# Kernel tuning notes

Measured on AMD Instinct MI355X. Metric: run time of the kernel, lower is better.

Reference implementation:

```python
import jax, jax.numpy as jnp
import numpy as np

D_MODEL = 512
NUM_HEADS = 8
D_HEAD = D_MODEL // NUM_HEADS
QMAX = 127.0  # int8 narrow-range symmetric
EPS = 1e-8


def _quant_dequant_weight(w):
    # per-output-channel symmetric int8 quant-dequant (brevitas default style)
    s = jnp.maximum(jnp.max(jnp.abs(w), axis=1, keepdims=True) / QMAX, EPS)
    return jnp.clip(jnp.round(w / s), -QMAX, QMAX) * s


def _quant_dequant_act(x):
    # per-tensor symmetric int8 quant-dequant (QuantIdentity)
    s = jnp.maximum(jnp.max(jnp.abs(x)) / QMAX, EPS)
    return jnp.clip(jnp.round(x / s), -QMAX, QMAX) * s


def _qlinear(x, w, b):
    return jnp.einsum('btd,od->bto', x, _quant_dequant_weight(w)) + b


def setup_inputs() -> dict:
    key = jax.random.key(0)
    ks = jax.random.split(key, 10)
    B, T = 2, 4096
    lim = 1.0 / np.sqrt(D_MODEL)
    mk = lambda k: jax.random.uniform(k, (D_MODEL, D_MODEL), jnp.float32, -lim, lim)
    mb = lambda k: jax.random.uniform(k, (D_MODEL,), jnp.float32, -lim, lim)
    return {
        'x': jax.random.normal(ks[0], (B, T, D_MODEL), jnp.float32),
        'mask': jax.random.randint(ks[1], (B, T), 0, 2, jnp.int32),
        'Wq': mk(ks[2]), 'bq': mb(ks[3]),
        'Wk': mk(ks[4]), 'bk': mb(ks[5]),
        'Wv': mk(ks[6]), 'bv': mb(ks[7]),
        'Wo': mk(ks[8]), 'bo': mb(ks[9]),
    }


def reference(x, mask, Wq, bq, Wk, bk, Wv, bv, Wo, bo):
    B, T, _ = x.shape
    shape = lambda t: t.reshape(B, T, NUM_HEADS, D_HEAD).transpose(0, 2, 1, 3)  # (B,H,T,dh)
    q = shape(_qlinear(x, Wq, bq))
    k = shape(_qlinear(x, Wk, bk))
    v = shape(_qlinear(x, Wv, bv))
    scores = jnp.einsum('bhtd,bhsd->bhts', q, k) / np.sqrt(D_HEAD)
    keep = (mask != 0)[:, None, None, :]  # (B,1,1,T), 0 = masked
    scores = jnp.where(keep, scores, -jnp.inf)
    attn = jax.nn.softmax(scores, axis=-1)
    ctx = jnp.einsum('bhts,bhsd->bhtd', attn, v)
    ctx = ctx.transpose(0, 2, 1, 3).reshape(B, T, D_MODEL)
    out = _qlinear(ctx, Wo, bo)
    return _quant_dequant_act(out)
```

## Files before the change

### kernel.cpp

```cpp
#include <hip/hip_runtime.h>
#include <hip/hip_bf16.h>

typedef __bf16 bf16;
typedef __bf16 bf16x8 __attribute__((ext_vector_type(8)));
typedef __bf16 bf16x4v __attribute__((ext_vector_type(4)));
typedef float f32x4 __attribute__((ext_vector_type(4)));

#define D_MODEL 512
#define T_SEQ   4096
#define NH      8
#define DH      64
#define M_ROWS  8192
#define VROW    8224
#define QK_SCALE 0.18033688011112042f

__device__ __forceinline__ void gload16(const void* g, void* l) {
  __builtin_amdgcn_global_load_lds(
      (const __attribute__((address_space(1))) unsigned int*)g,
      (__attribute__((address_space(3))) unsigned int*)l, 16, 0, 0);
}

#define WAITV(N) asm volatile("s_waitcnt vmcnt(" #N ")" ::: "memory")
#define CFENCE   asm volatile("" ::: "memory")

__global__ __launch_bounds__(64) void detect_dtype(const unsigned short* __restrict__ xr,
                                                   int* __restrict__ flag)
{
  int lane = threadIdx.x;
  int cnt = 0;
  for (int i = lane; i < 4096; i += 64) {
    unsigned short u = xr[i];
    int e = (u >> 7) & 0xFF;
    bool insane = (e >= 133) || (e > 0 && e <= 96) || (e == 0 && (u & 0x7F) != 0);
    cnt += insane ? 1 : 0;
  }
#pragma unroll
  for (int off = 32; off >= 1; off >>= 1) cnt += __shfl_xor(cnt, off);
  if (lane == 0) *flag = (cnt > 400) ? 1 : 0;
}

__global__ __launch_bounds__(256) void convert_x(const void* __restrict__ xr,
                                                 const int* __restrict__ flag,
                                                 bf16* __restrict__ xb, int n)
{
  int i = (blockIdx.x * blockDim.x + threadIdx.x) * 4;
  if (i >= n) return;
  if (*flag) {
    float4 v = *(const float4*)((const float*)xr + i);
    __align__(8) bf16 o[4] = {(bf16)v.x, (bf16)v.y, (bf16)v.z, (bf16)v.w};
    *(uint2*)(xb + i) = *(uint2*)o;
  } else {
    *(uint2*)(xb + i) = *(const uint2*)((const bf16*)xr + i);
  }
}

__global__ __launch_bounds__(1024) void prep_aux(
    const void* b0, const void* b1, const void* b2, const void* b3,
    const int* __restrict__ mask,
    const int* __restrict__ flag, float* __restrict__ bf, float* __restrict__ mf)
{
  const void* ps[4] = {b0, b1, b2, b3};
  int fl = *flag;
  int g = blockIdx.x * 1024 + threadIdx.x;
  if (g < 4 * D_MODEL) {
    int w = g >> 9, o = g & 511;
    bf[g] = fl ? ((const float*)ps[w])[o] : (float)((const bf16*)ps[w])[o];
  }
  mf[g] = mask[g] ? -16.0f : -1e30f;
}

__global__ __launch_bounds__(256) void qdq_weights(
    const void* __restrict__ Wq, const void* __restrict__ Wk,
    const void* __restrict__ Wv, const void* __restrict__ Wo,
    const int* __restrict__ flag, bf16* __restrict__ out)
{
  int wave = threadIdx.x >> 6, lane = threadIdx.x & 63;
  int gid = blockIdx.x * 4 + wave;
  int w = gid >> 9, row = gid & 511;
  const void* W = (w == 0) ? Wq : (w == 1) ? Wk : (w == 2) ? Wv : Wo;
  int fl = *flag;
  float v[8]; float amax = 0.f;
#pragma unroll
  for (int i = 0; i < 8; i++) {
    int idx = row * D_MODEL + lane + 64 * i;
    v[i] = fl ? ((const float*)W)[idx] : (float)((const bf16*)W)[idx];
    amax = fmaxf(amax, fabsf(v[i]));
  }
#pragma unroll
  for (int off = 32; off >= 1; off >>= 1) amax = fmaxf(amax, __shfl_xor(amax, off));
  float s = fmaxf(amax / 127.0f, 1e-8f);
  bf16* dst = out + (size_t)gid * D_MODEL;
#pragma unroll
  for (int i = 0; i < 8; i++) {
    float q = rintf(v[i] / s);
    q = fminf(fmaxf(q, -127.f), 127.f);
    dst[lane + 64*i] = (bf16)(q * s);
  }
}

__global__ __launch_bounds__(256) void gemm_qkv(
    const bf16* __restrict__ A, const bf16* __restrict__ W,
    const float* __restrict__ bias,
    bf16* __restrict__ Qh, bf16* __restrict__ Kh, bf16* __restrict__ VTP)
{
  __shared__ __align__(16) bf16 As[2][128 * 32];
  __shared__ __align__(16) bf16 Bs[2][128 * 32];

  const int tid = threadIdx.x;
  const int wave = tid >> 6, lane = tid & 63;
  const int lr = lane & 15, quad = lane >> 4;
  const int wm = (wave >> 1) * 64, wn = (wave & 1) * 64;
  const int m0 = blockIdx.x * 128, n0 = blockIdx.y * 128;
  const int sec = blockIdx.y >> 2;

  const bf16* aSrc[2]; const bf16* bSrc[2];
#pragma unroll
  for (int ii = 0; ii < 2; ii++) {
    int s = ii * 256 + tid, row = s >> 2, sl = s & 3;
    int g = (row ^ (row >> 2)) & 3;
    aSrc[ii] = A + (size_t)(m0 + row) * D_MODEL + ((sl ^ g) << 3);
    bSrc[ii] = W + (size_t)(n0 + row) * D_MODEL + ((sl ^ g) << 3);
  }

  f32x4 acc[4][4];
#pragma unroll
  for (int i = 0; i < 4; i++)
#pragma unroll
    for (int j = 0; j < 4; j++) acc[i][j] = f32x4{0.f, 0.f, 0.f, 0.f};

#pragma unroll
  for (int d = 0; d < 2; d++) {
#pragma unroll
    for (int ii = 0; ii < 2; ii++) {
      int s = ii * 256 + tid;
      gload16(aSrc[ii] + d * 32, &As[d][s * 8]);
      gload16(bSrc[ii] + d * 32, &Bs[d][s * 8]);
    }
  }
  WAITV(4);
  __builtin_amdgcn_s_barrier();
  CFENCE;

  for (int k = 0; k < 16; k++) {
    const int cur = k & 1;
    bf16x8 af[4], bfr[4];
#pragma unroll
    for (int mt = 0; mt < 4; mt++) {
      int row = wm + mt * 16 + lr;
      af[mt] = *(const bf16x8*)&As[cur][row * 32 + ((quad ^ ((row ^ (row >> 2)) & 3)) << 3)];
    }
#pragma unroll
    for (int nt = 0; nt < 4; nt++) {
      int row = wn + nt * 16 + lr;
      bfr[nt] = *(const bf16x8*)&Bs[cur][row * 32 + ((quad ^ ((row ^ (row >> 2)) & 3)) << 3)];
    }
#pragma unroll
    for (int mt = 0; mt < 4; mt++)
#pragma unroll
      for (int nt = 0; nt < 4; nt++)
        acc[mt][nt] = __builtin_amdgcn_mfma_f32_16x16x32_bf16(af[mt], bfr[nt], acc[mt][nt], 0, 0, 0);

    if (k < 15) {
      __builtin_amdgcn_s_barrier();
      CFENCE;
      if (k < 14) {
#pragma unroll
        for (int ii = 0; ii < 2; ii++) {
          int s = ii * 256 + tid;
          gload16(aSrc[ii] + (k + 2) * 32, &As[cur][s * 8]);
          gload16(bSrc[ii] + (k + 2) * 32, &Bs[cur][s * 8]);
        }
        WAITV(4);
      } else {
        WAITV(0);
      }
      __builtin_amdgcn_s_barrier();
      CFENCE;
    }
  }

  const float scale = (sec == 0) ? QK_SCALE : 1.0f;
#pragma unroll
  for (int mt = 0; mt < 4; mt++) {
    int grow = m0 + wm + mt * 16 + quad * 4;
#pragma unroll
    for (int nt = 0; nt < 4; nt++) {
      int gcol = n0 + wn + nt * 16 + lr;
      float b = bias[gcol];
      if (sec == 2) {
        bf16x4v pk;
#pragma unroll
        for (int r = 0; r < 4; r++) pk[r] = (bf16)(acc[mt][nt][r] + b);
        *(bf16x4v*)(VTP + (size_t)(gcol - 1024) * VROW + grow) = pk;
      } else {
        bf16* dst = (sec == 0) ? Qh : Kh;
        int c = gcol & 511;
        int hh = c >> 6, c64 = c & 63;
#pragma unroll
        for (int r = 0; r < 4; r++) {
          int row = grow + r;
          int bb = row >> 12, t = row & 4095;
          dst[((size_t)(bb * NH + hh) * T_SEQ + t) * DH + c64] =
              (bf16)((acc[mt][nt][r] + b) * scale);
        }
      }
    }
  }
}

__global__ __launch_bounds__(256) void gemm_o(
    const bf16* __restrict__ A, const bf16* __restrict__ W,
    const float* __restrict__ bias,
    float* __restrict__ Cf, unsigned int* __restrict__ amaxp)
{
  __shared__ __align__(16) bf16 As[2][64 * 32];
  __shared__ __align__(16) bf16 Bs[2][128 * 32];
  __shared__ float wred[4];

  const int tid = threadIdx.x;
  const int wave = tid >> 6, lane = tid & 63;
  const int lr = lane & 15, quad = lane >> 4;
  const int wm = (wave >> 1) * 32, wn = (wave & 1) * 64;
  const int m0 = blockIdx.x * 64, n0 = blockIdx.y * 128;

  const bf16* aSrc; const bf16* bSrc[2];
  {
    int s = tid, row = s >> 2, sl = s & 3;
    int g = (row ^ (row >> 2)) & 3;
    aSrc = A + (size_t)(m0 + row) * D_MODEL + ((sl ^ g) << 3);
  }
#pragma unroll
  for (int ii = 0; ii < 2; ii++) {
    int s = ii * 256 + tid, row = s >> 2, sl = s & 3;
    int g = (row ^ (row >> 2)) & 3;
    bSrc[ii] = W + (size_t)(n0 + row) * D_MODEL + ((sl ^ g) << 3);
  }

  f32x4 acc[2][4];
#pragma unroll
  for (int i = 0; i < 2; i++)
#pragma unroll
    for (int j = 0; j < 4; j++) acc[i][j] = f32x4{0.f, 0.f, 0.f, 0.f};

#pragma unroll
  for (int d = 0; d < 2; d++) {
    gload16(aSrc + d * 32, &As[d][tid * 8]);
#pragma unroll
    for (int ii = 0; ii < 2; ii++) {
      int s = ii * 256 + tid;
      gload16(bSrc[ii] + d * 32, &Bs[d][s * 8]);
    }
  }
  WAITV(3);
  __builtin_amdgcn_s_barrier();
  CFENCE;

  for (int k = 0; k < 16; k++) {
    const int cur = k & 1;
    bf16x8 af[2], bfr[4];
#pragma unroll
    for (int mt = 0; mt < 2; mt++) {
      int row = wm + mt * 16 + lr;
      af[mt] = *(const bf16x8*)&As[cur][row * 32 + ((quad ^ ((row ^ (row >> 2)) & 3)) << 3)];
    }
#pragma unroll
    for (int nt = 0; nt < 4; nt++) {
      int row = wn + nt * 16 + lr;
      bfr[nt] = *(const bf16x8*)&Bs[cur][row * 32 + ((quad ^ ((row ^ (row >> 2)) & 3)) << 3)];
    }
#pragma unroll
    for (int mt = 0; mt < 2; mt++)
#pragma unroll
      for (int nt = 0; nt < 4; nt++)
        acc[mt][nt] = __builtin_amdgcn_mfma_f32_16x16x32_bf16(af[mt], bfr[nt], acc[mt][nt], 0, 0, 0);

    if (k < 15) {
      __builtin_amdgcn_s_barrier();
      CFENCE;
      if (k < 14) {
        gload16(aSrc + (k + 2) * 32, &As[cur][tid * 8]);
#pragma unroll
        for (int ii = 0; ii < 2; ii++) {
          int s = ii * 256 + tid;
          gload16(bSrc[ii] + (k + 2) * 32, &Bs[cur][s * 8]);
        }
        WAITV(3);
      } else {
        WAITV(0);
      }
      __builtin_amdgcn_s_barrier();
      CFENCE;
    }
  }

  float lmax = 0.f;
#pragma unroll
  for (int mt = 0; mt < 2; mt++) {
    int grow = m0 + wm + mt * 16 + quad * 4;
#pragma unroll
    for (int nt = 0; nt < 4; nt++) {
      int gcol = n0 + wn + nt * 16 + lr;
      float b = bias[gcol];
#pragma unroll
      for (int r = 0; r < 4; r++) {
        float v = acc[mt][nt][r] + b;
        Cf[(size_t)(grow + r) * D_MODEL + gcol] = v;
        lmax = fmaxf(lmax, fabsf(v));
      }
    }
  }
#pragma unroll
  for (int off = 32; off >= 1; off >>= 1) lmax = fmaxf(lmax, __shfl_xor(lmax, off));
  if (lane == 0) wred[wave] = lmax;
  __syncthreads();
  if (tid == 0) {
    float m = fmaxf(fmaxf(wred[0], wred[1]), fmaxf(wred[2], wred[3]));
    atomicMax(amaxp, __float_as_uint(m));
  }
}

__global__ __launch_bounds__(256, 2) void attn(
    const bf16* __restrict__ Q, const bf16* __restrict__ K, const bf16* __restrict__ VT,
    const float* __restrict__ maskf, bf16* __restrict__ ctx)
{
  __shared__ __align__(16) bf16 Ks[3][64 * 64];
  __shared__ __align__(16) bf16 Vs[3][64 * 64];
  __shared__ __align__(16) float Mf[T_SEQ];

  const int tid = threadIdx.x;
  const int wave = tid >> 6, lane = tid & 63;
  const int lr = lane & 15, quad = lane >> 4;
  const int i = blockIdx.x;
  const int bh = (i & 7) * 2 + ((i >> 3) & 1);
  const int qb = i >> 4;
  const int b = bh >> 3, h = bh & 7;
  const int q0 = qb * 128 + wave * 32;

  const bf16* Qb = Q + (size_t)bh * T_SEQ * DH;
  const bf16* Kb = K + (size_t)bh * T_SEQ * DH;
  const bf16* Vb = VT + (size_t)(h * DH) * VROW + (size_t)b * T_SEQ;
  const float* mb = maskf + b * T_SEQ;

  const int phase = (qb * 2) & 63;

  const bf16* kSrc[2]; const bf16* vSrc[2];
#pragma unroll
  for (int ii = 0; ii < 2; ii++) {
    int s = ii * 256 + tid, row = s >> 3, sl = s & 7;
    int kt = row >> 4, m = row & 15;
    int keym = ((m >> 2) << 3) + ((kt & 1) << 2) + (m & 3) + ((kt >> 1) << 5);
    kSrc[ii] = Kb + (size_t)keym * DH + ((sl ^ (row & 7)) << 3);
    vSrc[ii] = Vb + (size_t)row * VROW + ((sl ^ (row & 7)) << 3);
  }

  bf16x8 qf[2][2];
#pragma unroll
  for (int qt = 0; qt < 2; qt++) {
    const bf16* rq = Qb + (size_t)(q0 + qt * 16 + lr) * DH;
    qf[qt][0] = *(const bf16x8*)(rq + quad * 8);
    qf[qt][1] = *(const bf16x8*)(rq + 32 + quad * 8);
  }
  WAITV(0);

#pragma unroll
  for (int ii = 0; ii < 4; ii++) {
    int g = ii * 256 + tid;
    gload16(mb + g * 4, &Mf[g * 4]);
  }
#pragma unroll
  for (int d = 0; d < 3; d++) {
    int kb = ((phase + d) & 63) * 64;
#pragma unroll
    for (int ii = 0; ii < 2; ii++) {
      int s = ii * 256 + tid;
      gload16(kSrc[ii] + (size_t)kb * DH, &Ks[d][s * 8]);
      gload16(vSrc[ii] + kb, &Vs[d][s * 8]);
    }
  }

  f32x4 O[2][4];
#pragma unroll
  for (int a = 0; a < 2; a++)
#pragma unroll
    for (int c = 0; c < 4; c++) O[a][c] = f32x4{0.f, 0.f, 0.f, 0.f};
  float lacc[2] = {0.f, 0.f};

  WAITV(8);
  __builtin_amdgcn_s_barrier();
  CFENCE;

  int cur = 0, cc = phase;
  for (int j = 0; j < 64; j++) {
    f32x4 mk[4];
#pragma unroll
    for (int kt = 0; kt < 4; kt++)
      mk[kt] = *(const f32x4*)&Mf[cc * 64 + ((kt >> 1) << 5) + (quad << 3) + ((kt & 1) << 2)];

    bf16x8 kr[4][2];
#pragma unroll
    for (int kt = 0; kt < 4; kt++)
#pragma unroll
      for (int kh = 0; kh < 2; kh++)
        kr[kt][kh] = *(const bf16x8*)&Ks[cur][(kt * 16 + lr) * 64 +
                                             (((kh * 4 + quad) ^ (lr & 7)) << 3)];

    bf16x8 pfa[2][2];
#pragma unroll
    for (int qt = 0; qt < 2; qt++) {
      f32x4 z[4];
#pragma unroll
      for (int kt = 0; kt < 4; kt++) {
        f32x4 t = mk[kt];
        t = __builtin_amdgcn_mfma_f32_16x16x32_bf16(kr[kt][0], qf[qt][0], t, 0, 0, 0);
        t = __builtin_amdgcn_mfma_f32_16x16x32_bf16(kr[kt][1], qf[qt][1], t, 0, 0, 0);
        z[kt] = t;
      }
      float la = lacc[qt];
#pragma unroll
      for (int kt = 0; kt < 4; kt++) {
#pragma unroll
        for (int r = 0; r < 4; r++) {
          float p = __builtin_amdgcn_exp2f(z[kt][r]);
          la += p;
          pfa[qt][kt >> 1][((kt & 1) << 2) + r] = (bf16)p;
        }
      }
      lacc[qt] = la;
    }

    bf16x8 vr[4][2];
#pragma unroll
    for (int nt = 0; nt < 4; nt++)
#pragma unroll
      for (int ks = 0; ks < 2; ks++)
        vr[nt][ks] = *(const bf16x8*)&Vs[cur][(nt * 16 + lr) * 64 +
                                             (((ks * 4 + quad) ^ (lr & 7)) << 3)];

#pragma unroll
    for (int nt = 0; nt < 4; nt++)
#pragma unroll
      for (int qt = 0; qt < 2; qt++) {
        O[qt][nt] = __builtin_amdgcn_mfma_f32_16x16x32_bf16(pfa[qt][0], vr[nt][0], O[qt][nt], 0, 0, 0);
        O[qt][nt] = __builtin_amdgcn_mfma_f32_16x16x32_bf16(pfa[qt][1], vr[nt][1], O[qt][nt], 0, 0, 0);
      }

    if (j < 63) {
      __builtin_amdgcn_s_barrier();
      CFENCE;
      if (j < 61) {
        int kb = ((cc + 3) & 63) * 64;
#pragma unroll
        for (int ii = 0; ii < 2; ii++) {
          int s = ii * 256 + tid;
          gload16(kSrc[ii] + (size_t)kb * DH, &Ks[cur][s * 8]);
          gload16(vSrc[ii] + kb, &Vs[cur][s * 8]);
        }
        WAITV(8);
      } else if (j == 61) {
        WAITV(4);
      } else {
        WAITV(0);
      }
      __builtin_amdgcn_s_barrier();
      CFENCE;
    }
    cur = (cur == 2) ? 0 : cur + 1;
    cc = (cc + 1) & 63;
  }

#pragma unroll
  for (int qt = 0; qt < 2; qt++) {
    float ls = lacc[qt];
    ls += __shfl_xor(ls, 16);
    ls += __shfl_xor(ls, 32);
    float linv = 1.0f / ls;
    float lO[4];
#pragma unroll
    for (int r = 0; r < 4; r++) lO[r] = __shfl(linv, quad * 4 + r);
#pragma unroll
    for (int nt = 0; nt < 4; nt++)
#pragma unroll
      for (int r = 0; r < 4; r++) {
        size_t row = (size_t)(b * T_SEQ + q0 + qt * 16 + quad * 4 + r);
        ctx[row * D_MODEL + h * DH + nt * 16 + lr] = (bf16)(O[qt][nt][r] * lO[r]);
      }
  }
}

__global__ __launch_bounds__(256) void act_qdq(
    const float* __restrict__ pre, const unsigned int* __restrict__ amaxp,
    const int* __restrict__ flag, void* __restrict__ outv, int n)
{
  int i = (blockIdx.x * blockDim.x + threadIdx.x) * 4;
  if (i >= n) return;
  float s = fmaxf(__uint_as_float(*amaxp) / 127.0f, 1e-8f);
  float4 v = *(const float4*)(pre + i);
  float o[4] = {v.x, v.y, v.z, v.w};
#pragma unroll
  for (int r = 0; r < 4; r++) {
    float q = rintf(o[r] / s);
    q = fminf(fmaxf(q, -127.f), 127.f);
    o[r] = q * s;
  }
  if (*flag) {
    *(float4*)((float*)outv + i) = make_float4(o[0], o[1], o[2], o[3]);
  } else {
    __align__(8) bf16 ob[4] = {(bf16)o[0], (bf16)o[1], (bf16)o[2], (bf16)o[3]};
    *(uint2*)((bf16*)outv + i) = *(uint2*)ob;
  }
}

extern "C" void kernel_launch(void* const* d_in, const int* in_sizes, int n_in,
                              void* d_out, int out_size, void* d_ws, size_t ws_size,
                              hipStream_t stream) {
  const void* x    = d_in[0];
  const int*  mask = (const int*)d_in[1];
  const void* Wq = d_in[2]; const void* bq = d_in[3];
  const void* Wk = d_in[4]; const void* bk = d_in[5];
  const void* Wv = d_in[6]; const void* bv = d_in[7];
  const void* Wo = d_in[8]; const void* bo = d_in[9];

  char* ws = (char*)d_ws;
  int*  flag  = (int*)(ws + 0);
  unsigned int* amax = (unsigned int*)(ws + 64);
  float* biasf = (float*)(ws + 1024);
  float* maskf = (float*)(ws + 16384);
  bf16* Wt  = (bf16*)(ws + 65536);
  bf16* xb  = (bf16*)(ws + 4194304);
  bf16* Qm  = (bf16*)(ws + 12582912);
  bf16* Km  = (bf16*)(ws + 20971520);
  bf16* VT  = (bf16*)(ws + 29360128);
  bf16* Cm  = (bf16*)(ws + 4194304);
  float* pre = (float*)(ws + 12582912);

  hipMemsetAsync(amax, 0, 4, stream);
  detect_dtype<<<1, 64, 0, stream>>>((const unsigned short*)x, flag);
  convert_x<<<4096, 256, 0, stream>>>(x, flag, xb, M_ROWS * D_MODEL);
  prep_aux<<<8, 1024, 0, stream>>>(bq, bk, bv, bo, mask, flag, biasf, maskf);
  qdq_weights<<<512, 256, 0, stream>>>(Wq, Wk, Wv, Wo, flag, Wt);
  gemm_qkv<<<dim3(64, 12), 256, 0, stream>>>(xb, Wt, biasf, Qm, Km, VT);
  attn<<<512, 256, 0, stream>>>(Qm, Km, VT, maskf, Cm);
  gemm_o<<<dim3(128, 4), 256, 0, stream>>>(Cm, Wt + 3*262144, biasf + 1536, pre, amax);
  act_qdq<<<4096, 256, 0, stream>>>(pre, amax, flag, d_out, M_ROWS * D_MODEL);
}
```

Before: 215.8 us.

## Fuse preprocessing kernels and transpose MFMA operands for vectorized Q/K stores

Merges the dtype detection, amax memset, bias/mask prep and weight quant-dequant into a single prep_all launch, where each block recomputes the dtype flag redundantly. This removes several small launches and a memset. In gemm_qkv, the Q/K sections swap the MFMA operands so each lane holds four consecutive head-dim columns, which lets the epilogue write packed 4-element bf16 stores instead of scalar ones. Every block now re-reads the first 4096 elements of x to compute the flag, which adds some redundant traffic.

Result: no change. 219.4 us (+1.7%).

```diff
diff --git a/kernel.cpp b/kernel.cpp
--- a/kernel.cpp
+++ b/kernel.cpp
@@ -23,12 +23,22 @@
 #define WAITV(N) asm volatile("s_waitcnt vmcnt(" #N ")" ::: "memory")
 #define CFENCE   asm volatile("" ::: "memory")
 
-__global__ __launch_bounds__(64) void detect_dtype(const unsigned short* __restrict__ xr,
-                                                   int* __restrict__ flag)
+__global__ __launch_bounds__(256) void prep_all(
+    const void* __restrict__ x, const int* __restrict__ mask,
+    const void* __restrict__ Wq, const void* __restrict__ Wk,
+    const void* __restrict__ Wv, const void* __restrict__ Wo,
+    const void* __restrict__ bq, const void* __restrict__ bk,
+    const void* __restrict__ bv, const void* __restrict__ bo,
+    bf16* __restrict__ out, float* __restrict__ bf, float* __restrict__ mf,
+    int* __restrict__ flag, unsigned int* __restrict__ amax)
 {
-  int lane = threadIdx.x;
+  __shared__ int wcnt[4];
+  __shared__ int sfl;
+  const int tid = threadIdx.x;
+  const unsigned short* xr = (const unsigned short*)x;
+
   int cnt = 0;
-  for (int i = lane; i < 4096; i += 64) {
+  for (int i = tid; i < 4096; i += 256) {
     unsigned short u = xr[i];
     int e = (u >> 7) & 0xFF;
     bool insane = (e >= 133) || (e > 0 && e <= 96) || (e == 0 && (u & 0x7F) != 0);
@@ -36,7 +46,52 @@
   }
 #pragma unroll
   for (int off = 32; off >= 1; off >>= 1) cnt += __shfl_xor(cnt, off);
-  if (lane == 0) *flag = (cnt > 400) ? 1 : 0;
+  if ((tid & 63) == 0) wcnt[tid >> 6] = cnt;
+  __syncthreads();
+  if (tid == 0) sfl = ((wcnt[0] + wcnt[1] + wcnt[2] + wcnt[3]) > 400) ? 1 : 0;
+  __syncthreads();
+  const int fl = sfl;
+
+  const int blk = blockIdx.x;
+  if (blk < 512) {
+    int wave = tid >> 6, lane = tid & 63;
+    int gid = blk * 4 + wave;
+    int w = gid >> 9, row = gid & 511;
+    const void* W = (w == 0) ? Wq : (w == 1) ? Wk : (w == 2) ? Wv : Wo;
+    float v[8]; float am = 0.f;
+#pragma unroll
+    for (int i = 0; i < 8; i++) {
+      int idx = row * D_MODEL + lane + 64 * i;
+      v[i] = fl ? ((const float*)W)[idx] : (float)((const bf16*)W)[idx];
+      am = fmaxf(am, fabsf(v[i]));
+    }
+#pragma unroll
+    for (int off = 32; off >= 1; off >>= 1) am = fmaxf(am, __shfl_xor(am, off));
+    float s = fmaxf(am / 127.0f, 1e-8f);
+    bf16* dst = out + (size_t)gid * D_MODEL;
+#pragma unroll
+    for (int i = 0; i < 8; i++) {
+      float q = rintf(v[i] / s);
+      q = fminf(fmaxf(q, -127.f), 127.f);
+      dst[lane + 64 * i] = (bf16)(q * s);
+    }
+  } else {
+    int ab = blk - 512;
+    int j = ab * 1024 + tid * 4;
+    int4 mv = *(const int4*)&mask[j];
+    mf[j + 0] = mv.x ? -16.0f : -1e30f;
+    mf[j + 1] = mv.y ? -16.0f : -1e30f;
+    mf[j + 2] = mv.z ? -16.0f : -1e30f;
+    mf[j + 3] = mv.w ? -16.0f : -1e30f;
+    if (ab == 0) {
+      const void* ps[4] = {bq, bk, bv, bo};
+      for (int t = tid; t < 4 * D_MODEL; t += 256) {
+        int w = t >> 9, o = t & 511;
+        bf[t] = fl ? ((const float*)ps[w])[o] : (float)((const bf16*)ps[w])[o];
+      }
+      if (tid == 0) { *flag = fl; *amax = 0u; }
+    }
+  }
 }
 
 __global__ __launch_bounds__(256) void convert_x(const void* __restrict__ xr,
@@ -54,50 +109,6 @@
   }
 }
 
-__global__ __launch_bounds__(1024) void prep_aux(
-    const void* b0, const void* b1, const void* b2, const void* b3,
-    const int* __restrict__ mask,
-    const int* __restrict__ flag, float* __restrict__ bf, float* __restrict__ mf)
-{
-  const void* ps[4] = {b0, b1, b2, b3};
-  int fl = *flag;
-  int g = blockIdx.x * 1024 + threadIdx.x;
-  if (g < 4 * D_MODEL) {
-    int w = g >> 9, o = g & 511;
-    bf[g] = fl ? ((const float*)ps[w])[o] : (float)((const bf16*)ps[w])[o];
-  }
-  mf[g] = mask[g] ? -16.0f : -1e30f;
-}
-
-__global__ __launch_bounds__(256) void qdq_weights(
-    const void* __restrict__ Wq, const void* __restrict__ Wk,
-    const void* __restrict__ Wv, const void* __restrict__ Wo,
-    const int* __restrict__ flag, bf16* __restrict__ out)
-{
-  int wave = threadIdx.x >> 6, lane = threadIdx.x & 63;
-  int gid = blockIdx.x * 4 + wave;
-  int w = gid >> 9, row = gid & 511;
-  const void* W = (w == 0) ? Wq : (w == 1) ? Wk : (w == 2) ? Wv : Wo;
-  int fl = *flag;
-  float v[8]; float amax = 0.f;
-#pragma unroll
-  for (int i = 0; i < 8; i++) {
-    int idx = row * D_MODEL + lane + 64 * i;
-    v[i] = fl ? ((const float*)W)[idx] : (float)((const bf16*)W)[idx];
-    amax = fmaxf(amax, fabsf(v[i]));
-  }
-#pragma unroll
-  for (int off = 32; off >= 1; off >>= 1) amax = fmaxf(amax, __shfl_xor(amax, off));
-  float s = fmaxf(amax / 127.0f, 1e-8f);
-  bf16* dst = out + (size_t)gid * D_MODEL;
-#pragma unroll
-  for (int i = 0; i < 8; i++) {
-    float q = rintf(v[i] / s);
-    q = fminf(fmaxf(q, -127.f), 127.f);
-    dst[lane + 64*i] = (bf16)(q * s);
-  }
-}
-
 __global__ __launch_bounds__(256) void gemm_qkv(
     const bf16* __restrict__ A, const bf16* __restrict__ W,
     const float* __restrict__ bias,
@@ -154,11 +165,19 @@
       int row = wn + nt * 16 + lr;
       bfr[nt] = *(const bf16x8*)&Bs[cur][row * 32 + ((quad ^ ((row ^ (row >> 2)) & 3)) << 3)];
     }
-#pragma unroll
-    for (int mt = 0; mt < 4; mt++)
-#pragma unroll
-      for (int nt = 0; nt < 4; nt++)
-        acc[mt][nt] = __builtin_amdgcn_mfma_f32_16x16x32_bf16(af[mt], bfr[nt], acc[mt][nt], 0, 0, 0);
+    if (sec == 2) {
+#pragma unroll
+      for (int mt = 0; mt < 4; mt++)
+#pragma unroll
+        for (int nt = 0; nt < 4; nt++)
+          acc[mt][nt] = __builtin_amdgcn_mfma_f32_16x16x32_bf16(af[mt], bfr[nt], acc[mt][nt], 0, 0, 0);
+    } else {
+#pragma unroll
+      for (int mt = 0; mt < 4; mt++)
+#pragma unroll
+        for (int nt = 0; nt < 4; nt++)
+          acc[nt][mt] = __builtin_amdgcn_mfma_f32_16x16x32_bf16(bfr[nt], af[mt], acc[nt][mt], 0, 0, 0);
+    }
 
     if (k < 15) {
       __builtin_amdgcn_s_barrier();
@@ -179,30 +198,37 @@
     }
   }
 
-  const float scale = (sec == 0) ? QK_SCALE : 1.0f;
-#pragma unroll
-  for (int mt = 0; mt < 4; mt++) {
-    int grow = m0 + wm + mt * 16 + quad * 4;
-#pragma unroll
-    for (int nt = 0; nt < 4; nt++) {
-      int gcol = n0 + wn + nt * 16 + lr;
-      float b = bias[gcol];
-      if (sec == 2) {
+  if (sec == 2) {
+#pragma unroll
+    for (int mt = 0; mt < 4; mt++) {
+      int grow = m0 + wm + mt * 16 + quad * 4;
+#pragma unroll
+      for (int nt = 0; nt < 4; nt++) {
+        int gcol = n0 + wn + nt * 16 + lr;
+        float b = bias[gcol];
         bf16x4v pk;
 #pragma unroll
         for (int r = 0; r < 4; r++) pk[r] = (bf16)(acc[mt][nt][r] + b);
         *(bf16x4v*)(VTP + (size_t)(gcol - 1024) * VROW + grow) = pk;
-      } else {
-        bf16* dst = (sec == 0) ? Qh : Kh;
-        int c = gcol & 511;
-        int hh = c >> 6, c64 = c & 63;
-#pragma unroll
-        for (int r = 0; r < 4; r++) {
-          int row = grow + r;
-          int bb = row >> 12, t = row & 4095;
-          dst[((size_t)(bb * NH + hh) * T_SEQ + t) * DH + c64] =
-              (bf16)((acc[mt][nt][r] + b) * scale);
-        }
+      }
+    }
+  } else {
+    const float scale = (sec == 0) ? QK_SCALE : 1.0f;
+    bf16* dst = (sec == 0) ? Qh : Kh;
+#pragma unroll
+    for (int i = 0; i < 4; i++) {
+      int cbase = n0 + wn + i * 16 + quad * 4;
+      int c = cbase & 511;
+      int hh = c >> 6, c64 = c & 63;
+      f32x4 bv = *(const f32x4*)&bias[cbase];
+#pragma unroll
+      for (int j = 0; j < 4; j++) {
+        int row = m0 + wm + j * 16 + lr;
+        int bb = row >> 12, t = row & 4095;
+        bf16x4v pk;
+#pragma unroll
+        for (int r = 0; r < 4; r++) pk[r] = (bf16)((acc[i][j][r] + bv[r]) * scale);
+        *(bf16x4v*)(dst + ((size_t)(bb * NH + hh) * T_SEQ + t) * DH + c64) = pk;
       }
     }
   }
@@ -533,11 +559,9 @@
   bf16* Cm  = (bf16*)(ws + 4194304);
   float* pre = (float*)(ws + 12582912);
 
-  hipMemsetAsync(amax, 0, 4, stream);
-  detect_dtype<<<1, 64, 0, stream>>>((const unsigned short*)x, flag);
+  prep_all<<<520, 256, 0, stream>>>(x, mask, Wq, Wk, Wv, Wo, bq, bk, bv, bo,
+                                    Wt, biasf, maskf, flag, amax);
   convert_x<<<4096, 256, 0, stream>>>(x, flag, xb, M_ROWS * D_MODEL);
-  prep_aux<<<8, 1024, 0, stream>>>(bq, bk, bv, bo, mask, flag, biasf, maskf);
-  qdq_weights<<<512, 256, 0, stream>>>(Wq, Wk, Wv, Wo, flag, Wt);
   gemm_qkv<<<dim3(64, 12), 256, 0, stream>>>(xb, Wt, biasf, Qm, Km, VT);
   attn<<<512, 256, 0, stream>>>(Qm, Km, VT, maskf, Cm);
   gemm_o<<<dim3(128, 4), 256, 0, stream>>>(Cm, Wt + 3*262144, biasf + 1536, pre, amax);
```
